# Kernel optimization log

Hardware: AMD Instinct MI355X
Metric: run time of the kernel (lower is better)

The kernel has to match this reference:

```python
import jax, jax.numpy as jnp
import numpy as np

B, T, D_IN, H, K, C = 8, 2048, 512, 384, 8192, 8
N_BLOCKS = 6
EPS = 1e-5


def conv1d(x, w, b, pad, groups=1):
    # x: [B, Cin, T], w: [Cout, Cin//groups, k]
    y = jax.lax.conv_general_dilated(
        x, w, window_strides=(1,), padding=[(pad, pad)],
        dimension_numbers=("NCH", "OIH", "NCH"), feature_group_count=groups)
    return y + b[None, :, None]


def layernorm(x, g, b):
    # normalize over last axis
    m = jnp.mean(x, axis=-1, keepdims=True)
    v = jnp.mean(jnp.square(x - m), axis=-1, keepdims=True)
    return (x - m) * jax.lax.rsqrt(v + EPS) * g + b


def setup_inputs() -> dict:
    key = jax.random.key(0)
    ks = iter(jax.random.split(key, 32))
    s = 0.02
    inp = {
        "x": jax.random.normal(next(ks), (B, T, D_IN), dtype=jnp.float32),
        "enc_w": jax.random.normal(next(ks), (H, D_IN, 7)) * s,
        "enc_b": jnp.zeros((H,)),
        "enc_ln_g": jnp.ones((H,)),
        "enc_ln_b": jnp.zeros((H,)),
        "blk_dw_w": jax.random.normal(next(ks), (N_BLOCKS, H, 1, 7)) * s,
        "blk_dw_b": jnp.zeros((N_BLOCKS, H)),
        "blk_ln_g": jnp.ones((N_BLOCKS, H)),
        "blk_ln_b": jnp.zeros((N_BLOCKS, H)),
        "blk_w1": jax.random.normal(next(ks), (N_BLOCKS, 4 * H, H)) * s,
        "blk_b1": jnp.zeros((N_BLOCKS, 4 * H)),
        "blk_w2": jax.random.normal(next(ks), (N_BLOCKS, H, 4 * H)) * s,
        "blk_b2": jnp.zeros((N_BLOCKS, H)),
        "out_w": jax.random.normal(next(ks), (C, H, 1)) * s,
        "out_b": jnp.zeros((C,)),
        "embeddings": jax.random.normal(next(ks), (K, C)),
    }
    return inp


def encode(x, enc_w, enc_b, enc_ln_g, enc_ln_b, blk_dw_w, blk_dw_b,
           blk_ln_g, blk_ln_b, blk_w1, blk_b1, blk_w2, blk_b2, out_w, out_b):
    h = x.transpose(0, 2, 1)                       # [B, D_IN, T]
    h = conv1d(h, enc_w, enc_b, pad=3)             # [B, H, T]
    h = layernorm(h.transpose(0, 2, 1), enc_ln_g, enc_ln_b).transpose(0, 2, 1)
    for i in range(N_BLOCKS):
        res = h
        h = conv1d(h, blk_dw_w[i], blk_dw_b[i], pad=3, groups=H)  # depthwise
        ht = h.transpose(0, 2, 1)                  # [B, T, H]
        ht = layernorm(ht, blk_ln_g[i], blk_ln_b[i])
        ht = jnp.einsum("bth,fh->btf", ht, blk_w1[i]) + blk_b1[i]
        ht = jax.nn.gelu(ht, approximate=False)    # torch GELU is exact erf
        ht = jnp.einsum("btf,hf->bth", ht, blk_w2[i]) + blk_b2[i]
        h = ht.transpose(0, 2, 1) + res
    z = conv1d(h, out_w, out_b, pad=0)             # [B, C, T]
    return z.transpose(0, 2, 1)                    # [B, T, C]


def reference(x, enc_w, enc_b, enc_ln_g, enc_ln_b, blk_dw_w, blk_dw_b,
              blk_ln_g, blk_ln_b, blk_w1, blk_b1, blk_w2, blk_b2,
              out_w, out_b, embeddings):
    z = encode(x, enc_w, enc_b, enc_ln_g, enc_ln_b, blk_dw_w, blk_dw_b,
               blk_ln_g, blk_ln_b, blk_w1, blk_b1, blk_w2, blk_b2, out_w, out_b)
    flat = z.reshape(-1, C)                        # [B*T, C]
    # squared euclidean distances: same argmin as torch.cdist
    d2 = (jnp.sum(flat * flat, axis=1, keepdims=True)
          - 2.0 * flat @ embeddings.T
          + jnp.sum(embeddings * embeddings, axis=1))  # [B*T, K]
    indices = jnp.argmin(d2, axis=1)               # [B*T], int
    return indices
```

## Files before the change

kernel.cpp:

```cpp
#include <hip/hip_runtime.h>
#include <math.h>

#define T_   2048
#define DIN  512
#define H_   384
#define H4_  1536
#define BT_  16384

typedef _Float16 half_t;
typedef _Float16 f16x8 __attribute__((ext_vector_type(8)));
typedef float f32x4 __attribute__((ext_vector_type(4)));

#define LO_SCALE 2048.0f
#define LO_INV   4.8828125e-4f

#define APLANE 4096
#define ASL_OFF 8192
#define BSH_OFF 16384
#define BSL_OFF 24576
#define SMEM_H  32768

__device__ __forceinline__ void lds_barrier() {
    asm volatile("s_waitcnt lgkmcnt(0)\n\ts_barrier" ::: "memory");
}

__device__ __forceinline__ void split2(float v, half_t* hi, half_t* lo) {
    half_t h = (half_t)v;
    *hi = h;
    *lo = (half_t)((v - (float)h) * LO_SCALE);
}

__global__ void k_split(const float* __restrict__ in, half_t* __restrict__ hi,
                        half_t* __restrict__ lo, long n) {
    long i = (long)blockIdx.x * 256 + threadIdx.x;
    if (i >= n) return;
    split2(in[i], hi + i, lo + i);
}

__global__ void k_split_encw(const float* __restrict__ in, half_t* __restrict__ hi,
                             half_t* __restrict__ lo) {
    int idx = blockIdx.x * 256 + threadIdx.x;
    if (idx >= H_ * 3584) return;
    int n = idx / 3584;
    int r = idx % 3584;
    int tap = r >> 9, i = r & 511;
    split2(in[n * 3584 + i * 7 + tap], hi + idx, lo + idx);
}

__global__ void k_ln(const float* __restrict__ in, float* __restrict__ out,
                     const float* __restrict__ g, const float* __restrict__ b) {
    int row = blockIdx.x;
    int lane = threadIdx.x;
    const float* ir = in + (long)row * H_;
    float v[6];
    float s = 0.f;
#pragma unroll
    for (int j = 0; j < 6; ++j) { v[j] = ir[lane + (j << 6)]; s += v[j]; }
#pragma unroll
    for (int o = 32; o > 0; o >>= 1) s += __shfl_down(s, o, 64);
    s = __shfl(s, 0, 64);
    float mean = s * (1.f / 384.f);
    float q = 0.f;
#pragma unroll
    for (int j = 0; j < 6; ++j) { float d = v[j] - mean; q += d * d; }
#pragma unroll
    for (int o = 32; o > 0; o >>= 1) q += __shfl_down(q, o, 64);
    q = __shfl(q, 0, 64);
    float rstd = rsqrtf(q * (1.f / 384.f) + 1e-5f);
    float* orow = out + (long)row * H_;
#pragma unroll
    for (int j = 0; j < 6; ++j) {
        int c = lane + (j << 6);
        orow[c] = (v[j] - mean) * rstd * g[c] + b[c];
    }
}

__global__ __launch_bounds__(256) void k_dwconv_ln(
    const float* __restrict__ h, half_t* __restrict__ oh,
    half_t* __restrict__ ol,
    const float* __restrict__ w, const float* __restrict__ wb,
    const float* __restrict__ g, const float* __restrict__ gb) {
    int row = (blockIdx.x << 2) + (threadIdx.x >> 6);
    int b = row >> 11;
    int t = row & 2047;
    int lane = threadIdx.x & 63;
    const float* hb = h + ((long)b * T_) * H_;
    float v[6];
    float s = 0.f;
#pragma unroll
    for (int j = 0; j < 6; ++j) {
        int c = lane + (j << 6);
        float acc = wb[c];
        const float* wc = w + c * 7;
#pragma unroll
        for (int k = 0; k < 7; ++k) {
            int tt = t + k - 3;
            if ((unsigned)tt < (unsigned)T_)
                acc = fmaf(hb[(long)tt * H_ + c], wc[k], acc);
        }
        v[j] = acc;
        s += acc;
    }
#pragma unroll
    for (int o = 32; o > 0; o >>= 1) s += __shfl_down(s, o, 64);
    s = __shfl(s, 0, 64);
    float mean = s * (1.f / 384.f);
    float q = 0.f;
#pragma unroll
    for (int j = 0; j < 6; ++j) { float d = v[j] - mean; q += d * d; }
#pragma unroll
    for (int o = 32; o > 0; o >>= 1) q += __shfl_down(q, o, 64);
    q = __shfl(q, 0, 64);
    float rstd = rsqrtf(q * (1.f / 384.f) + 1e-5f);
    long ro = (long)row * H_;
#pragma unroll
    for (int j = 0; j < 6; ++j) {
        int c = lane + (j << 6);
        float val = (v[j] - mean) * rstd * g[c] + gb[c];
        split2(val, oh + ro + c, ol + ro + c);
    }
}

template <int MODE>
__global__ __launch_bounds__(512) void k_mgemm(
    const half_t* __restrict__ Ah, const half_t* __restrict__ Al,
    const half_t* __restrict__ Bh, const half_t* __restrict__ Bl,
    const float* __restrict__ bias, const float* __restrict__ res,
    float* __restrict__ Cf, half_t* __restrict__ Ch, half_t* __restrict__ Cl,
    int N, int K) {
    __shared__ __align__(16) half_t smem[SMEM_H];
    const int tid = threadIdx.x;
    const int lane = tid & 63, wid = tid >> 6;
    const int wm = (wid >> 2) << 6, wn = (wid & 3) << 5;
    const int quad = lane >> 4, l16 = lane & 15;
    const int m0 = (MODE == 0 ? blockIdx.x : blockIdx.y) << 7;
    const int n0 = (MODE == 0 ? blockIdx.y : blockIdx.x) << 7;
    const int ar = tid >> 2;
    const int ak = (tid & 3) << 3;

    long aoff = 0;
    int tt0 = 0, bq = 0;
    if (MODE == 0) {
        bq = m0 >> 11;
        tt0 = (m0 & 2047) + ar - 3;
    } else {
        aoff = (long)(m0 + ar) * K + ak;
    }
    const long boff = (long)(n0 + ar) * K + ak;

    float4 pAh, pAl, pBh, pBl;
    auto loadregs = [&](int k0) {
        if (MODE == 0) {
            int kk = k0 + ak;
            int tap = kk >> 9, ii = kk & 511;
            int ta = tt0 + tap;
            pAh = pAl = make_float4(0.f, 0.f, 0.f, 0.f);
            if ((unsigned)ta < 2048u) {
                long o = ((long)bq * 2048 + ta) * 512 + ii;
                pAh = *(const float4*)(Ah + o);
                pAl = *(const float4*)(Al + o);
            }
        } else {
            pAh = *(const float4*)(Ah + aoff + k0);
            pAl = *(const float4*)(Al + aoff + k0);
        }
        pBh = *(const float4*)(Bh + boff + k0);
        pBl = *(const float4*)(Bl + boff + k0);
    };
    const int aw = ar * 32 + ((((tid & 3) ^ ar) & 3) << 3);
    auto storebuf = [&](int buf) {
        int a = buf * APLANE + aw;
        *(float4*)&smem[a] = pAh;
        *(float4*)&smem[a + ASL_OFF] = pAl;
        *(float4*)&smem[a + BSH_OFF] = pBh;
        *(float4*)&smem[a + BSL_OFF] = pBl;
    };

    f32x4 acc1[4][2] = {};
    f32x4 acc2[4][2] = {};

    loadregs(0);
    storebuf(0);
    const int nIter = K >> 5;
    int cur = 0;
    const int sw = ((quad ^ l16) & 3) << 3;
    for (int it = 0; it < nIter; ++it) {
        if (it + 1 < nIter) loadregs((it + 1) << 5);
        lds_barrier();
        const int ab = cur * APLANE + (wm + l16) * 32 + sw;
        const int bb = BSH_OFF + cur * APLANE + (wn + l16) * 32 + sw;
        f16x8 fah[4], fal[4], fgh[2], fgl[2];
#pragma unroll
        for (int f = 0; f < 4; ++f) {
            fah[f] = *(const f16x8*)&smem[ab + f * 512];
            fal[f] = *(const f16x8*)&smem[ab + ASL_OFF + f * 512];
        }
#pragma unroll
        for (int g = 0; g < 2; ++g) {
            fgh[g] = *(const f16x8*)&smem[bb + g * 512];
            fgl[g] = *(const f16x8*)&smem[bb + ASL_OFF + g * 512];
        }
#pragma unroll
        for (int f = 0; f < 4; ++f)
#pragma unroll
            for (int g = 0; g < 2; ++g)
                acc2[f][g] = __builtin_amdgcn_mfma_f32_16x16x32_f16(fah[f], fgl[g], acc2[f][g], 0, 0, 0);
#pragma unroll
        for (int f = 0; f < 4; ++f)
#pragma unroll
            for (int g = 0; g < 2; ++g)
                acc2[f][g] = __builtin_amdgcn_mfma_f32_16x16x32_f16(fal[f], fgh[g], acc2[f][g], 0, 0, 0);
#pragma unroll
        for (int f = 0; f < 4; ++f)
#pragma unroll
            for (int g = 0; g < 2; ++g)
                acc1[f][g] = __builtin_amdgcn_mfma_f32_16x16x32_f16(fah[f], fgh[g], acc1[f][g], 0, 0, 0);
        if (it + 1 < nIter) storebuf(cur ^ 1);
        cur ^= 1;
    }

    float bv[2];
    bv[0] = bias[n0 + wn + l16];
    bv[1] = bias[n0 + wn + 16 + l16];

    if (MODE == 1) {
#pragma unroll
        for (int h2 = 0; h2 < 2; ++h2) {
            __syncthreads();
            if (((wid >> 1) & 1) == h2) {
                int cbase = (wid & 1) << 5;
#pragma unroll
                for (int f = 0; f < 4; ++f)
#pragma unroll
                    for (int g = 0; g < 2; ++g)
#pragma unroll
                        for (int r = 0; r < 4; ++r) {
                            int rm = wm + f * 16 + quad * 4 + r;
                            int cn = cbase + g * 16 + l16;
                            float v = acc1[f][g][r] + acc2[f][g][r] * LO_INV + bv[g];
                            v = 0.5f * v * (1.0f + erff(v * 0.70710678118654752f));
                            half_t hh = (half_t)v;
                            smem[rm * 72 + cn] = hh;
                            smem[9216 + rm * 72 + cn] = (half_t)((v - (float)hh) * LO_SCALE);
                        }
            }
            __syncthreads();
            int row = tid >> 2, c16 = (tid & 3) << 4;
            long go = (long)(m0 + row) * N + n0 + (h2 << 6) + c16;
            *(float4*)(Ch + go)     = *(const float4*)&smem[row * 72 + c16];
            *(float4*)(Ch + go + 8) = *(const float4*)&smem[row * 72 + c16 + 8];
            *(float4*)(Cl + go)     = *(const float4*)&smem[9216 + row * 72 + c16];
            *(float4*)(Cl + go + 8) = *(const float4*)&smem[9216 + row * 72 + c16 + 8];
        }
    } else {
#pragma unroll
        for (int f = 0; f < 4; ++f)
#pragma unroll
            for (int g = 0; g < 2; ++g)
#pragma unroll
                for (int r = 0; r < 4; ++r) {
                    long row = m0 + wm + f * 16 + quad * 4 + r;
                    int col = n0 + wn + g * 16 + l16;
                    float v = acc1[f][g][r] + acc2[f][g][r] * LO_INV + bv[g];
                    long o = row * N + col;
                    if (MODE == 2) v += res[o];
                    Cf[o] = v;
                }
    }
}

__global__ __launch_bounds__(256) void k_outconv_argmin(
    const float* __restrict__ h, const float* __restrict__ ow,
    const float* __restrict__ ob, const float* __restrict__ emb,
    int* __restrict__ outIdx) {
    __shared__ float hs[16][H_ + 1];
    __shared__ float zs[16][8];
    __shared__ float es[16 * 516];
    __shared__ float rb[16][16];
    __shared__ int ri[16][16];
    const int tid = threadIdx.x;
    const int row0 = blockIdx.x << 4;

    for (int i = tid; i < 16 * (H_ / 4); i += 256) {
        int r = i / 96;
        int c4 = (i % 96) << 2;
        float4 v = *(const float4*)&h[((long)(row0 + r)) * H_ + c4];
        hs[r][c4] = v.x; hs[r][c4 + 1] = v.y; hs[r][c4 + 2] = v.z; hs[r][c4 + 3] = v.w;
    }
    __syncthreads();

    if (tid < 128) {
        int r = tid & 15, c = tid >> 4;
        float acc = ob[c];
        const float* wc = ow + c * H_;
        for (int j = 0; j < H_; ++j) acc = fmaf(hs[r][j], wc[j], acc);
        zs[r][c] = acc;
    }
    __syncthreads();

    const int r = tid & 15;
    const int sl = tid >> 4;
    float z0 = zs[r][0], z1 = zs[r][1], z2 = zs[r][2], z3 = zs[r][3];
    float z4 = zs[r][4], z5 = zs[r][5], z6 = zs[r][6], z7 = zs[r][7];
    float best = 3.4e38f;
    int bi = 0;

    for (int ch = 0; ch < 8; ++ch) {
        __syncthreads();
        for (int i = tid; i < 2048; i += 256) {
            int e = i >> 1;
            int half = (i & 1) << 2;
            float4 src = *(const float4*)&emb[(((long)(ch << 10)) + e) * 8 + half];
            *(float4*)&es[(e >> 6) * 516 + ((e & 63) << 3) + half] = src;
        }
        __syncthreads();
        const float* ep = es + sl * 516;
        int gbase = (ch << 10) + (sl << 6);
#pragma unroll 4
        for (int j = 0; j < 64; ++j) {
            float4 e0 = *(const float4*)(ep + (j << 3));
            float4 e1 = *(const float4*)(ep + (j << 3) + 4);
            float t, d;
            t = e0.x - z0; d = t * t;
            t = e0.y - z1; d = fmaf(t, t, d);
            t = e0.z - z2; d = fmaf(t, t, d);
            t = e0.w - z3; d = fmaf(t, t, d);
            t = e1.x - z4; d = fmaf(t, t, d);
            t = e1.y - z5; d = fmaf(t, t, d);
            t = e1.z - z6; d = fmaf(t, t, d);
            t = e1.w - z7; d = fmaf(t, t, d);
            if (d < best) { best = d; bi = gbase + j; }
        }
    }
    rb[r][sl] = best;
    ri[r][sl] = bi;
    __syncthreads();
    if (sl == 0) {
        float bb = rb[r][0];
        int bbi = ri[r][0];
#pragma unroll
        for (int s2 = 1; s2 < 16; ++s2) {
            float v = rb[r][s2];
            int i2 = ri[r][s2];
            if (v < bb || (v == bb && i2 < bbi)) { bb = v; bbi = i2; }
        }
        outIdx[row0 + r] = bbi;
    }
}

extern "C" void kernel_launch(void* const* d_in, const int* in_sizes, int n_in,
                              void* d_out, int out_size, void* d_ws, size_t ws_size,
                              hipStream_t stream) {
    const float* x        = (const float*)d_in[0];
    const float* enc_w    = (const float*)d_in[1];
    const float* enc_b    = (const float*)d_in[2];
    const float* enc_ln_g = (const float*)d_in[3];
    const float* enc_ln_b = (const float*)d_in[4];
    const float* blk_dw_w = (const float*)d_in[5];
    const float* blk_dw_b = (const float*)d_in[6];
    const float* blk_ln_g = (const float*)d_in[7];
    const float* blk_ln_b = (const float*)d_in[8];
    const float* blk_w1   = (const float*)d_in[9];
    const float* blk_b1   = (const float*)d_in[10];
    const float* blk_w2   = (const float*)d_in[11];
    const float* blk_b2   = (const float*)d_in[12];
    const float* out_w    = (const float*)d_in[13];
    const float* out_b    = (const float*)d_in[14];
    const float* emb      = (const float*)d_in[15];
    int* out = (int*)d_out;

    char* base = (char*)d_ws;
    float*  h    = (float*)base;
    half_t* tmph = (half_t*)(base + 25165824);
    half_t* tmpl = (half_t*)(base + 37748736);
    half_t* ht4h = (half_t*)(base + 50331648);
    half_t* ht4l = (half_t*)(base + 100663296);
    half_t* ench = (half_t*)(base + 150994944);
    half_t* encl = (half_t*)(base + 153747456);
    half_t* w1h  = (half_t*)(base + 156499968);
    half_t* w1l  = (half_t*)(base + 163577856);
    half_t* w2h  = (half_t*)(base + 170655744);
    half_t* w2l  = (half_t*)(base + 177733632);
    half_t* xh = ht4h;
    half_t* xl = (half_t*)(base + 50331648 + 16777216);

    k_split<<<(8388608 + 255) / 256, 256, 0, stream>>>(x, xh, xl, 8388608L);
    k_split<<<(3538944 + 255) / 256, 256, 0, stream>>>(blk_w1, w1h, w1l, 3538944L);
    k_split<<<(3538944 + 255) / 256, 256, 0, stream>>>(blk_w2, w2h, w2l, 3538944L);
    k_split_encw<<<(H_ * 3584 + 255) / 256, 256, 0, stream>>>(enc_w, ench, encl);

    k_mgemm<0><<<dim3(128, 3), 512, 0, stream>>>(xh, xl, ench, encl, enc_b,
                                                 nullptr, h, nullptr, nullptr,
                                                 H_, 3584);
    k_ln<<<BT_, 64, 0, stream>>>(h, h, enc_ln_g, enc_ln_b);

    for (int i = 0; i < 6; ++i) {
        k_dwconv_ln<<<BT_ / 4, 256, 0, stream>>>(h, tmph, tmpl, blk_dw_w + i * H_ * 7,
                                                 blk_dw_b + i * H_, blk_ln_g + i * H_,
                                                 blk_ln_b + i * H_);
        k_mgemm<1><<<dim3(12, 128), 512, 0, stream>>>(
            tmph, tmpl, w1h + (long)i * 589824, w1l + (long)i * 589824,
            blk_b1 + i * H4_, nullptr, nullptr, ht4h, ht4l, H4_, H_);
        k_mgemm<2><<<dim3(3, 128), 512, 0, stream>>>(
            ht4h, ht4l, w2h + (long)i * 589824, w2l + (long)i * 589824,
            blk_b2 + i * H_, h, h, nullptr, nullptr, H_, H4_);
    }

    k_outconv_argmin<<<BT_ / 16, 256, 0, stream>>>(h, out_w, out_b, emb, out);
}
```

Baseline: 1.850 ms.

## Use 64x128-tile GEMM for narrow-N encoder and second MLP GEMMs

Splits the templated GEMM into a dedicated GELU-epilogue kernel for the wide first MLP projection and a new 256-thread 64x128-tile kernel for the encoder conv and second projection (N=384). This doubles the number of workgroups for those launches, from 384 to 768, to fill more CUs on a chip with many compute units. In exchange, each block reuses the B tile across fewer rows, so more weight traffic is read per FLOP.

```diff
diff --git a/kernel.cpp b/kernel.cpp
--- a/kernel.cpp
+++ b/kernel.cpp
@@ -13,12 +13,6 @@
 
 #define LO_SCALE 2048.0f
 #define LO_INV   4.8828125e-4f
-
-#define APLANE 4096
-#define ASL_OFF 8192
-#define BSH_OFF 16384
-#define BSL_OFF 24576
-#define SMEM_H  32768
 
 __device__ __forceinline__ void lds_barrier() {
     asm volatile("s_waitcnt lgkmcnt(0)\n\ts_barrier" ::: "memory");
@@ -122,19 +116,17 @@
 }
 
 template <int MODE>
-__global__ __launch_bounds__(512) void k_mgemm(
+__global__ __launch_bounds__(256) void k_mgemm64(
     const half_t* __restrict__ Ah, const half_t* __restrict__ Al,
     const half_t* __restrict__ Bh, const half_t* __restrict__ Bl,
     const float* __restrict__ bias, const float* __restrict__ res,
-    float* __restrict__ Cf, half_t* __restrict__ Ch, half_t* __restrict__ Cl,
-    int N, int K) {
-    __shared__ __align__(16) half_t smem[SMEM_H];
+    float* __restrict__ Cf, int N, int K) {
+    __shared__ __align__(16) half_t smem[24576];
     const int tid = threadIdx.x;
     const int lane = tid & 63, wid = tid >> 6;
-    const int wm = (wid >> 2) << 6, wn = (wid & 3) << 5;
+    const int wn = wid << 5;
     const int quad = lane >> 4, l16 = lane & 15;
-    const int m0 = (MODE == 0 ? blockIdx.x : blockIdx.y) << 7;
-    const int n0 = (MODE == 0 ? blockIdx.y : blockIdx.x) << 7;
+    const int m0 = blockIdx.x << 6, n0 = blockIdx.y << 7;
     const int ar = tid >> 2;
     const int ak = (tid & 3) << 3;
 
@@ -146,9 +138,10 @@
     } else {
         aoff = (long)(m0 + ar) * K + ak;
     }
-    const long boff = (long)(n0 + ar) * K + ak;
-
-    float4 pAh, pAl, pBh, pBl;
+    const long boff0 = (long)(n0 + ar) * K + ak;
+    const long boff1 = boff0 + (long)64 * K;
+
+    float4 pAh, pAl, pBh0, pBl0, pBh1, pBl1;
     auto loadregs = [&](int k0) {
         if (MODE == 0) {
             int kk = k0 + ak;
@@ -164,6 +157,110 @@
             pAh = *(const float4*)(Ah + aoff + k0);
             pAl = *(const float4*)(Al + aoff + k0);
         }
+        pBh0 = *(const float4*)(Bh + boff0 + k0);
+        pBl0 = *(const float4*)(Bl + boff0 + k0);
+        pBh1 = *(const float4*)(Bh + boff1 + k0);
+        pBl1 = *(const float4*)(Bl + boff1 + k0);
+    };
+    const int aw = ar * 32 + ((((tid & 3) ^ ar) & 3) << 3);
+    auto storebuf = [&](int buf) {
+        *(float4*)&smem[buf * 2048 + aw] = pAh;
+        *(float4*)&smem[4096 + buf * 2048 + aw] = pAl;
+        int b = 8192 + buf * 4096 + aw;
+        *(float4*)&smem[b] = pBh0;
+        *(float4*)&smem[b + 2048] = pBh1;
+        *(float4*)&smem[b + 8192] = pBl0;
+        *(float4*)&smem[b + 8192 + 2048] = pBl1;
+    };
+
+    f32x4 acc1[4][2] = {};
+    f32x4 acc2[4][2] = {};
+
+    loadregs(0);
+    storebuf(0);
+    const int nIter = K >> 5;
+    int cur = 0;
+    const int sw = ((quad ^ l16) & 3) << 3;
+    for (int it = 0; it < nIter; ++it) {
+        if (it + 1 < nIter) loadregs((it + 1) << 5);
+        lds_barrier();
+        const int ab = cur * 2048 + l16 * 32 + sw;
+        const int bb = 8192 + cur * 4096 + (wn + l16) * 32 + sw;
+        f16x8 fah[4], fal[4], fgh[2], fgl[2];
+#pragma unroll
+        for (int f = 0; f < 4; ++f) {
+            fah[f] = *(const f16x8*)&smem[ab + f * 512];
+            fal[f] = *(const f16x8*)&smem[ab + 4096 + f * 512];
+        }
+#pragma unroll
+        for (int g = 0; g < 2; ++g) {
+            fgh[g] = *(const f16x8*)&smem[bb + g * 512];
+            fgl[g] = *(const f16x8*)&smem[bb + 8192 + g * 512];
+        }
+#pragma unroll
+        for (int f = 0; f < 4; ++f)
+#pragma unroll
+            for (int g = 0; g < 2; ++g)
+                acc2[f][g] = __builtin_amdgcn_mfma_f32_16x16x32_f16(fah[f], fgl[g], acc2[f][g], 0, 0, 0);
+#pragma unroll
+        for (int f = 0; f < 4; ++f)
+#pragma unroll
+            for (int g = 0; g < 2; ++g)
+                acc2[f][g] = __builtin_amdgcn_mfma_f32_16x16x32_f16(fal[f], fgh[g], acc2[f][g], 0, 0, 0);
+#pragma unroll
+        for (int f = 0; f < 4; ++f)
+#pragma unroll
+            for (int g = 0; g < 2; ++g)
+                acc1[f][g] = __builtin_amdgcn_mfma_f32_16x16x32_f16(fah[f], fgh[g], acc1[f][g], 0, 0, 0);
+        if (it + 1 < nIter) storebuf(cur ^ 1);
+        cur ^= 1;
+    }
+
+    float bv[2];
+    bv[0] = bias[n0 + wn + l16];
+    bv[1] = bias[n0 + wn + 16 + l16];
+
+#pragma unroll
+    for (int f = 0; f < 4; ++f)
+#pragma unroll
+        for (int g = 0; g < 2; ++g)
+#pragma unroll
+            for (int r = 0; r < 4; ++r) {
+                long row = m0 + f * 16 + quad * 4 + r;
+                int col = n0 + wn + g * 16 + l16;
+                float v = acc1[f][g][r] + acc2[f][g][r] * LO_INV + bv[g];
+                long o = row * N + col;
+                if (MODE == 2) v += res[o];
+                Cf[o] = v;
+            }
+}
+
+#define APLANE 4096
+#define ASL_OFF 8192
+#define BSH_OFF 16384
+#define BSL_OFF 24576
+
+__global__ __launch_bounds__(512) void k_mgemm1(
+    const half_t* __restrict__ Ah, const half_t* __restrict__ Al,
+    const half_t* __restrict__ Bh, const half_t* __restrict__ Bl,
+    const float* __restrict__ bias,
+    half_t* __restrict__ Ch, half_t* __restrict__ Cl, int N, int K) {
+    __shared__ __align__(16) half_t smem[32768];
+    const int tid = threadIdx.x;
+    const int lane = tid & 63, wid = tid >> 6;
+    const int wm = (wid >> 2) << 6, wn = (wid & 3) << 5;
+    const int quad = lane >> 4, l16 = lane & 15;
+    const int m0 = blockIdx.y << 7, n0 = blockIdx.x << 7;
+    const int ar = tid >> 2;
+    const int ak = (tid & 3) << 3;
+
+    const long aoff = (long)(m0 + ar) * K + ak;
+    const long boff = (long)(n0 + ar) * K + ak;
+
+    float4 pAh, pAl, pBh, pBl;
+    auto loadregs = [&](int k0) {
+        pAh = *(const float4*)(Ah + aoff + k0);
+        pAl = *(const float4*)(Al + aoff + k0);
         pBh = *(const float4*)(Bh + boff + k0);
         pBl = *(const float4*)(Bl + boff + k0);
     };
@@ -223,49 +320,33 @@
     bv[0] = bias[n0 + wn + l16];
     bv[1] = bias[n0 + wn + 16 + l16];
 
-    if (MODE == 1) {
-#pragma unroll
-        for (int h2 = 0; h2 < 2; ++h2) {
-            __syncthreads();
-            if (((wid >> 1) & 1) == h2) {
-                int cbase = (wid & 1) << 5;
-#pragma unroll
-                for (int f = 0; f < 4; ++f)
-#pragma unroll
-                    for (int g = 0; g < 2; ++g)
-#pragma unroll
-                        for (int r = 0; r < 4; ++r) {
-                            int rm = wm + f * 16 + quad * 4 + r;
-                            int cn = cbase + g * 16 + l16;
-                            float v = acc1[f][g][r] + acc2[f][g][r] * LO_INV + bv[g];
-                            v = 0.5f * v * (1.0f + erff(v * 0.70710678118654752f));
-                            half_t hh = (half_t)v;
-                            smem[rm * 72 + cn] = hh;
-                            smem[9216 + rm * 72 + cn] = (half_t)((v - (float)hh) * LO_SCALE);
-                        }
-            }
-            __syncthreads();
-            int row = tid >> 2, c16 = (tid & 3) << 4;
-            long go = (long)(m0 + row) * N + n0 + (h2 << 6) + c16;
-            *(float4*)(Ch + go)     = *(const float4*)&smem[row * 72 + c16];
-            *(float4*)(Ch + go + 8) = *(const float4*)&smem[row * 72 + c16 + 8];
-            *(float4*)(Cl + go)     = *(const float4*)&smem[9216 + row * 72 + c16];
-            *(float4*)(Cl + go + 8) = *(const float4*)&smem[9216 + row * 72 + c16 + 8];
-        }
-    } else {
-#pragma unroll
-        for (int f = 0; f < 4; ++f)
-#pragma unroll
-            for (int g = 0; g < 2; ++g)
-#pragma unroll
-                for (int r = 0; r < 4; ++r) {
-                    long row = m0 + wm + f * 16 + quad * 4 + r;
-                    int col = n0 + wn + g * 16 + l16;
-                    float v = acc1[f][g][r] + acc2[f][g][r] * LO_INV + bv[g];
-                    long o = row * N + col;
-                    if (MODE == 2) v += res[o];
-                    Cf[o] = v;
-                }
+#pragma unroll
+    for (int h2 = 0; h2 < 2; ++h2) {
+        __syncthreads();
+        if (((wid >> 1) & 1) == h2) {
+            int cbase = (wid & 1) << 5;
+#pragma unroll
+            for (int f = 0; f < 4; ++f)
+#pragma unroll
+                for (int g = 0; g < 2; ++g)
+#pragma unroll
+                    for (int r = 0; r < 4; ++r) {
+                        int rm = wm + f * 16 + quad * 4 + r;
+                        int cn = cbase + g * 16 + l16;
+                        float v = acc1[f][g][r] + acc2[f][g][r] * LO_INV + bv[g];
+                        v = 0.5f * v * (1.0f + erff(v * 0.70710678118654752f));
+                        half_t hh = (half_t)v;
+                        smem[rm * 72 + cn] = hh;
+                        smem[9216 + rm * 72 + cn] = (half_t)((v - (float)hh) * LO_SCALE);
+                    }
+        }
+        __syncthreads();
+        int row = tid >> 2, c16 = (tid & 3) << 4;
+        long go = (long)(m0 + row) * N + n0 + (h2 << 6) + c16;
+        *(float4*)(Ch + go)     = *(const float4*)&smem[row * 72 + c16];
+        *(float4*)(Ch + go + 8) = *(const float4*)&smem[row * 72 + c16 + 8];
+        *(float4*)(Cl + go)     = *(const float4*)&smem[9216 + row * 72 + c16];
+        *(float4*)(Cl + go + 8) = *(const float4*)&smem[9216 + row * 72 + c16 + 8];
     }
 }
 
@@ -389,21 +470,20 @@
     k_split<<<(3538944 + 255) / 256, 256, 0, stream>>>(blk_w2, w2h, w2l, 3538944L);
     k_split_encw<<<(H_ * 3584 + 255) / 256, 256, 0, stream>>>(enc_w, ench, encl);
 
-    k_mgemm<0><<<dim3(128, 3), 512, 0, stream>>>(xh, xl, ench, encl, enc_b,
-                                                 nullptr, h, nullptr, nullptr,
-                                                 H_, 3584);
+    k_mgemm64<0><<<dim3(256, 3), 256, 0, stream>>>(xh, xl, ench, encl, enc_b,
+                                                   nullptr, h, H_, 3584);
     k_ln<<<BT_, 64, 0, stream>>>(h, h, enc_ln_g, enc_ln_b);
 
     for (int i = 0; i < 6; ++i) {
         k_dwconv_ln<<<BT_ / 4, 256, 0, stream>>>(h, tmph, tmpl, blk_dw_w + i * H_ * 7,
                                                  blk_dw_b + i * H_, blk_ln_g + i * H_,
                                                  blk_ln_b + i * H_);
-        k_mgemm<1><<<dim3(12, 128), 512, 0, stream>>>(
+        k_mgemm1<<<dim3(12, 128), 512, 0, stream>>>(
             tmph, tmpl, w1h + (long)i * 589824, w1l + (long)i * 589824,
-            blk_b1 + i * H4_, nullptr, nullptr, ht4h, ht4l, H4_, H_);
-        k_mgemm<2><<<dim3(3, 128), 512, 0, stream>>>(
+            blk_b1 + i * H4_, ht4h, ht4l, H4_, H_);
+        k_mgemm64<2><<<dim3(256, 3), 256, 0, stream>>>(
             ht4h, ht4l, w2h + (long)i * 589824, w2l + (long)i * 589824,
-            blk_b2 + i * H_, h, h, nullptr, nullptr, H_, H4_);
+            blk_b2 + i * H_, h, h, H_, H4_);
     }
 
     k_outconv_argmin<<<BT_ / 16, 256, 0, stream>>>(h, out_w, out_b, emb, out);
```

New measurement: 1.843 ms. Within noise of the previous version (-0.4%).
